# Kernel optimization log

Hardware: AMD Instinct MI355X
Metric: run time of the kernel (lower is better)

The kernel has to match this reference:

```python
import jax, jax.numpy as jnp
import numpy as np
from jax import lax

DIM = 128
N_WORD = 10000
N_FP = 100000
WINDOW = 5
KS = 2 * WINDOW + 1
L_GNN = 3
L_CNN = 3
L_OUT = 2
B, N_ATOM, L_PROT = 64, 256, 2048


def setup_inputs() -> dict:
    key = jax.random.key(0)
    ks = jax.random.split(key, 20)
    s = 0.1  # weight scale (module uses a custom weights_init; any small init is fine)
    return {
        "fingerprints": jax.random.randint(ks[0], (B, N_ATOM), 0, N_FP),
        "adjacency": jax.random.uniform(ks[1], (B, N_ATOM, N_ATOM), jnp.float32),
        "words": jax.random.randint(ks[2], (B, L_PROT), 0, N_WORD),
        "cmask": jnp.ones((B, N_ATOM), jnp.float32),
        "pmask": jnp.ones((B, L_PROT), jnp.float32),
        "label": jax.random.normal(ks[3], (B, 1), jnp.float32),
        "emb_fp": jax.random.normal(ks[4], (N_FP, DIM), jnp.float32) * s,
        "emb_word": jax.random.normal(ks[5], (N_WORD, DIM), jnp.float32) * s,
        "Wg": jax.random.normal(ks[6], (L_GNN, DIM, DIM), jnp.float32) * s,
        "bg": jax.random.normal(ks[7], (L_GNN, DIM), jnp.float32) * s,
        "Wc": jax.random.normal(ks[8], (L_CNN, 1, 1, KS, KS), jnp.float32) * s,
        "bc": jax.random.normal(ks[9], (L_CNN,), jnp.float32) * s,
        "Wa": jax.random.normal(ks[10], (DIM, DIM), jnp.float32) * s,
        "ba": jax.random.normal(ks[11], (DIM,), jnp.float32) * s,
        "Wo": jax.random.normal(ks[12], (L_OUT, 2 * DIM, 2 * DIM), jnp.float32) * s,
        "bo": jax.random.normal(ks[13], (L_OUT, 2 * DIM), jnp.float32) * s,
        "Wi": jax.random.normal(ks[14], (1, 2 * DIM), jnp.float32) * s,
        "bi": jax.random.normal(ks[15], (1,), jnp.float32) * s,
    }


def _conv2d(x, k, b):
    # x: [B,1,L,D], k: [1,1,KS,KS] -> same-padded conv, scalar bias
    y = lax.conv_general_dilated(x, k, (1, 1), [(WINDOW, WINDOW), (WINDOW, WINDOW)],
                                 dimension_numbers=("NCHW", "OIHW", "NCHW"))
    return y + b


def reference(fingerprints, adjacency, words, cmask, pmask, label,
              emb_fp, emb_word, Wg, bg, Wc, bc, Wa, ba, Wo, bo, Wi, bi):
    # --- GNN over compound graph ---
    xs = emb_fp[fingerprints]                          # [B,N,D]
    for i in range(L_GNN):
        hs = jax.nn.relu(jnp.einsum("bnd,ed->bne", xs, Wg[i]) + bg[i])
        xs = xs + jnp.matmul(adjacency, hs)            # residual message passing
    cm = cmask[:, :, None]
    compound = jnp.sum(xs * cm, axis=1) / jnp.sum(cm, axis=1)   # [B,D]

    # --- attention-CNN over protein words ---
    wv = emb_word[words]                               # [B,L,D]
    x4 = wv[:, None, :, :]                             # [B,1,L,D]
    for i in range(L_CNN):
        x4 = jax.nn.relu(_conv2d(x4, Wc[i], bc[i]))
    xs_p = x4[:, 0]                                    # [B,L,D]
    h = jax.nn.relu(compound @ Wa.T + ba)              # [B,D]
    hs = jax.nn.relu(jnp.einsum("bld,ed->ble", xs_p, Wa) + ba)  # [B,L,D]
    weights = jnp.tanh(jnp.einsum("bld,bd->bl", hs, h))[:, :, None]  # [B,L,1]
    ys = weights * hs
    pm = pmask[:, :, None]
    protein = jnp.sum(ys * pm, axis=1) / jnp.sum(pm, axis=1)    # [B,D]

    # --- output head ---
    cat = jnp.concatenate([compound, protein], axis=1)  # [B,2D]
    for j in range(L_OUT):
        cat = jax.nn.relu(cat @ Wo[j].T + bo[j])
    affinity = cat @ Wi.T + bi                           # [B,1]
    loss = jnp.mean((affinity - label) ** 2)             # MSELoss, weight 1
    return (loss, affinity)
```

## Files before the change

kernel.cpp:

```cpp
#include <hip/hip_runtime.h>
#include <hip/hip_bf16.h>
#include <math.h>

#define DIM   128
#define NA    256
#define NB    64
#define LPROT 2048
#define KSZ   11

#define TROWS   64
#define NTILES  (LPROT / TROWS)
#define FRS     152
#define XRS     136
#define B0_ROWS 106
#define B1_ROWS 96

typedef __attribute__((ext_vector_type(8))) short short8v;
typedef __attribute__((ext_vector_type(4))) short short4v;
typedef __attribute__((ext_vector_type(4))) float float4v;

__device__ inline unsigned short f2bf(float f) {
  __hip_bfloat16 h = __float2bfloat16(f);
  unsigned short u; __builtin_memcpy(&u, &h, 2); return u;
}
__device__ inline float bf2f(unsigned short s) {
  union { unsigned u; float f; } v; v.u = ((unsigned)s) << 16;
  return v.f;
}
__device__ inline short8v cvt8(const float* p) {
  float4 x = *(const float4*)p, y = *(const float4*)(p + 4);
  short8v t;
  t[0] = (short)f2bf(x.x); t[1] = (short)f2bf(x.y);
  t[2] = (short)f2bf(x.z); t[3] = (short)f2bf(x.w);
  t[4] = (short)f2bf(y.x); t[5] = (short)f2bf(y.y);
  t[6] = (short)f2bf(y.z); t[7] = (short)f2bf(y.w);
  return t;
}

#define HSTR 512
#define WSTR 256
__device__ inline int hta(int e, int nb) { return (e * HSTR + nb) ^ ((e & 7) << 4); }
__device__ inline int wga(int e, int cb) { return (e * WSTR + cb) ^ ((e & 7) << 4); }

__global__ __launch_bounds__(256) void k_cvtA(const float* __restrict__ A,
                                              unsigned short* __restrict__ Abf) {
  long i = ((long)blockIdx.x * 256 + threadIdx.x) * 8;
  *(short8v*)(Abf + i) = cvt8(A + i);
}

__global__ void k_prepw(const float* __restrict__ Wc, long* __restrict__ wbf) {
  int t = threadIdx.x;
  int lp = t >> 6, lane = t & 63;
  int lj = lane & 15, k0 = (lane >> 4) * 8;
  int bbase = 15 + k0 - lj;
  for (int ki = 0; ki < KSZ; ++ki) {
    float wr[8];
    #pragma unroll
    for (int i = 0; i < 8; ++i) {
      int t2 = bbase + i - 18;
      wr[i] = (t2 >= 0 && t2 < KSZ) ? Wc[lp * KSZ * KSZ + ki * KSZ + t2] : 0.f;
    }
    int lo = __builtin_amdgcn_cvt_pk_fp8_f32(wr[0], wr[1], 0, false);
    lo = __builtin_amdgcn_cvt_pk_fp8_f32(wr[2], wr[3], lo, true);
    int hi = __builtin_amdgcn_cvt_pk_fp8_f32(wr[4], wr[5], 0, false);
    hi = __builtin_amdgcn_cvt_pk_fp8_f32(wr[6], wr[7], hi, true);
    wbf[(lp * 64 + lane) * KSZ + ki] = ((long)hi << 32) | (unsigned)lo;
  }
}

template <bool GATHER>
__global__ __launch_bounds__(512, 2) void k_hs(const float* __restrict__ xs_in,
                                               const int* __restrict__ fp,
                                               const float* __restrict__ emb,
                                               const float* __restrict__ Wgl,
                                               const float* __restrict__ bgl,
                                               unsigned short* __restrict__ hsT) {
  __shared__ __align__(16) char wgp[128 * WSTR];
  const int blk = blockIdx.x, b = blk >> 2, q = blk & 3;
  const int tid = threadIdx.x, lane = tid & 63, w = tid >> 6;
  const int lj = lane & 15, g = lane >> 4, k0 = g * 8;

  for (int i = tid; i < 128 * 16; i += 512) {
    int row = i >> 4, c8 = (i & 15) * 8;
    *(short8v*)(wgp + wga(row, c8 * 2)) = cvt8(&Wgl[row * DIM + c8]);
  }

  const int rrow = q * 64 + (w >> 1) * 16 + lj;
  const int c0 = (w & 1) * 64;

  short8v afr[4];
  {
    const float* src;
    if (GATHER) src = &emb[(long)fp[b * NA + rrow] * DIM];
    else        src = &xs_in[((long)b * NA + rrow) * DIM];
    #pragma unroll
    for (int ks = 0; ks < 4; ++ks) afr[ks] = cvt8(src + ks * 32 + k0);
  }
  __syncthreads();

  float4v acc[4];
  #pragma unroll
  for (int c = 0; c < 4; ++c) acc[c] = (float4v){0.f, 0.f, 0.f, 0.f};
  #pragma unroll
  for (int ks = 0; ks < 4; ++ks)
    #pragma unroll
    for (int c = 0; c < 4; ++c) {
      short8v bf = *(const short8v*)(wgp + wga(c0 + c * 16 + lj, ks * 64 + g * 16));
      acc[c] = __builtin_amdgcn_mfma_f32_16x16x32_bf16(afr[ks], bf, acc[c], 0, 0, 0);
    }

  const int n0 = q * 64 + (w >> 1) * 16 + g * 4;
  #pragma unroll
  for (int c = 0; c < 4; ++c) {
    int e = c0 + c * 16 + lj;
    float bias = bgl[e];
    short4v s;
    #pragma unroll
    for (int jj = 0; jj < 4; ++jj)
      s[jj] = (short)f2bf(fmaxf(acc[c][jj] + bias, 0.f));
    *(short4v*)&hsT[((long)b * DIM + e) * NA + n0] = s;
  }
}

template <bool GATHER, bool LAST>
__global__ __launch_bounds__(512, 2) void k_adj(const float* __restrict__ xs_in,
                                                const int* __restrict__ fp,
                                                const float* __restrict__ emb,
                                                const unsigned short* __restrict__ Abf,
                                                const unsigned short* __restrict__ hsT,
                                                const float* __restrict__ cmask,
                                                float* __restrict__ xs_out,
                                                float* __restrict__ cred) {
  __shared__ __align__(16) char hl[128 * HSTR];
  const int blk = blockIdx.x, b = blk >> 2, q = blk & 3;
  const int tid = threadIdx.x, lane = tid & 63, w = tid >> 6;
  const int lj = lane & 15, g = lane >> 4, k0 = g * 8;

  for (int i = tid; i < 128 * 32; i += 512) {
    int row = i >> 5, c8 = (i & 31) * 8;
    *(short8v*)(hl + hta(row, c8 * 2)) =
        *(const short8v*)&hsT[((long)b * DIM + row) * NA + c8];
  }
  __syncthreads();

  const int wr = w >> 2, wc = w & 3;
  const int row0 = q * 64 + wr * 32;

  float4v acc[2][2];
  #pragma unroll
  for (int m = 0; m < 2; ++m)
    #pragma unroll
    for (int c = 0; c < 2; ++c) acc[m][c] = (float4v){0.f, 0.f, 0.f, 0.f};

  #pragma unroll 2
  for (int ks = 0; ks < 8; ++ks) {
    short8v af0 = *(const short8v*)
        &Abf[((long)b * NA + row0 + lj) * NA + ks * 32 + k0];
    short8v af1 = *(const short8v*)
        &Abf[((long)b * NA + row0 + 16 + lj) * NA + ks * 32 + k0];
    #pragma unroll
    for (int c = 0; c < 2; ++c) {
      short8v bf = *(const short8v*)(hl + hta(wc * 32 + c * 16 + lj, ks * 64 + g * 16));
      acc[0][c] = __builtin_amdgcn_mfma_f32_16x16x32_bf16(af0, bf, acc[0][c], 0, 0, 0);
      acc[1][c] = __builtin_amdgcn_mfma_f32_16x16x32_bf16(af1, bf, acc[1][c], 0, 0, 0);
    }
  }

  if (!LAST) {
    #pragma unroll
    for (int m = 0; m < 2; ++m)
      #pragma unroll
      for (int jj = 0; jj < 4; ++jj) {
        int row = row0 + m * 16 + g * 4 + jj;
        long base = ((long)b * NA + row) * DIM;
        const float* oldsrc;
        long gbase;
        if (GATHER) { gbase = (long)fp[b * NA + row] * DIM; oldsrc = emb; }
        else { gbase = base; oldsrc = xs_in; }
        #pragma unroll
        for (int c = 0; c < 2; ++c) {
          int col = wc * 32 + c * 16 + lj;
          xs_out[base + col] = oldsrc[gbase + col] + acc[m][c][jj];
        }
      }
  } else {
    float p[2] = {0.f, 0.f};
    #pragma unroll
    for (int m = 0; m < 2; ++m)
      #pragma unroll
      for (int jj = 0; jj < 4; ++jj) {
        int row = row0 + m * 16 + g * 4 + jj;
        float cm = cmask[b * NA + row];
        long base = ((long)b * NA + row) * DIM;
        #pragma unroll
        for (int c = 0; c < 2; ++c) {
          int col = wc * 32 + c * 16 + lj;
          float xv = xs_in[base + col] + acc[m][c][jj];
          p[c] = fmaf(xv, cm, p[c]);
        }
      }
    #pragma unroll
    for (int c = 0; c < 2; ++c) {
      p[c] += __shfl_xor(p[c], 16);
      p[c] += __shfl_xor(p[c], 32);
      if (g == 0)
        cred[((long)b * 8 + q * 2 + wr) * DIM + wc * 32 + c * 16 + lj] = p[c];
    }
  }
}

__global__ __launch_bounds__(128) void k_hv(const float* __restrict__ cred,
                                            const float* __restrict__ cmask,
                                            const float* __restrict__ Wa,
                                            const float* __restrict__ ba,
                                            float* __restrict__ compound,
                                            float* __restrict__ hv) {
  int b = blockIdx.x, e = threadIdx.x;
  __shared__ float comp[DIM];
  __shared__ float redm[DIM];
  float s = 0.f;
  #pragma unroll
  for (int p = 0; p < 8; ++p) s += cred[((long)b * 8 + p) * DIM + e];
  redm[e] = cmask[b * NA + e] + cmask[b * NA + DIM + e];
  __syncthreads();
  for (int st = 64; st > 0; st >>= 1) {
    if (e < st) redm[e] += redm[e + st];
    __syncthreads();
  }
  float c = s / redm[0];
  compound[b * DIM + e] = c;
  comp[e] = c;
  __syncthreads();
  float acc = 0.f;
  for (int d = 0; d < DIM; d += 4) {
    float4 wv = *(const float4*)&Wa[e * DIM + d];
    float4 x  = *(const float4*)&comp[d];
    acc = fmaf(x.x, wv.x, fmaf(x.y, wv.y, fmaf(x.z, wv.z, fmaf(x.w, wv.w, acc))));
  }
  hv[b * DIM + e] = fmaxf(acc + ba[e], 0.f);
}

template <bool ROWCHK, bool BF16OUT>
__device__ inline void conv_epi(const float4v& acc, int rc,
                                char* __restrict__ dst,
                                unsigned short* __restrict__ dstX,
                                float bias, int dstart, int lane, int cc) {
  const int lj = lane & 15;
  int orow = rc * 16 + (lane >> 4) * 4;
  int ocol = cc * 16 + lj;
  #pragma unroll
  for (int jj = 0; jj < 4; ++jj) {
    float v = fmaxf(acc[jj] + bias, 0.f);
    if constexpr (BF16OUT) {
      dstX[(orow + jj) * XRS + ocol] = f2bf(v);
    } else {
      char sv = 0;
      if (!ROWCHK || (unsigned)(dstart + orow + jj) < LPROT) {
        int p = __builtin_amdgcn_cvt_pk_fp8_f32(v, 0.f, 0, false);
        sv = (char)p;
      }
      dst[(orow + jj) * FRS + 8 + ocol] = sv;
    }
  }
}

template <int N_RC, bool ROWCHK, bool BF16OUT>
__device__ inline void conv_fp8(const char* __restrict__ src, char* __restrict__ dst,
                                unsigned short* __restrict__ dstX,
                                const long* bfr, float bias, int dstart,
                                int lane, int cc) {
  const int lj = lane & 15, k0 = (lane >> 4) * 8;
  const int acol = 8 + cc * 16 + k0;
  #pragma unroll 1
  for (int rp = 0; rp < N_RC / 2; ++rp) {
    const int rc0 = rp * 2, rc1 = rc0 + 1;
    float4v acc0 = {0.f, 0.f, 0.f, 0.f};
    float4v acc1 = {0.f, 0.f, 0.f, 0.f};
    #pragma unroll
    for (int ki = 0; ki < KSZ; ++ki) {
      long a0 = *(const long*)(src + (rc0 * 16 + lj + ki) * FRS + acol);
      long a1 = *(const long*)(src + (rc1 * 16 + lj + ki) * FRS + acol);
      acc0 = __builtin_amdgcn_mfma_f32_16x16x32_fp8_fp8(a0, bfr[ki], acc0, 0, 0, 0);
      acc1 = __builtin_amdgcn_mfma_f32_16x16x32_fp8_fp8(a1, bfr[ki], acc1, 0, 0, 0);
    }
    conv_epi<ROWCHK, BF16OUT>(acc0, rc0, dst, dstX, bias, dstart, lane, cc);
    conv_epi<ROWCHK, BF16OUT>(acc1, rc1, dst, dstX, bias, dstart, lane, cc);
  }
  if (N_RC & 1) {
    const int rc = N_RC - 1;
    float4v acc = {0.f, 0.f, 0.f, 0.f};
    #pragma unroll
    for (int ki = 0; ki < KSZ; ++ki) {
      long a = *(const long*)(src + (rc * 16 + lj + ki) * FRS + acol);
      acc = __builtin_amdgcn_mfma_f32_16x16x32_fp8_fp8(a, bfr[ki], acc, 0, 0, 0);
    }
    conv_epi<ROWCHK, BF16OUT>(acc, rc, dst, dstX, bias, dstart, lane, cc);
  }
}

__global__ __launch_bounds__(512, 6) void k_protein(const int* __restrict__ words,
                                                    const float* __restrict__ emb_word,
                                                    const long* __restrict__ wbf,
                                                    const float* __restrict__ bc,
                                                    const float* __restrict__ Wa,
                                                    const float* __restrict__ ba,
                                                    const float* __restrict__ hvec,
                                                    const float* __restrict__ pmask,
                                                    float* __restrict__ prot_part) {
  __shared__ __align__(16) char pool[48640];
  char* buf0 = pool;
  char* buf1 = pool + 16128;
  unsigned short* bufX = (unsigned short*)(pool + 30720);
  float* h_s  = (float*)(pool + 48128);
  float* wpart = (float*)(pool + 16128);
  float* w_l   = (float*)(pool + 16128 + 2048);
  float* red   = (float*)(pool + 16128 + 2304);

  const int tile = blockIdx.x, b = blockIdx.y;
  const int r0   = tile * TROWS;
  const int tid  = threadIdx.x;
  const int lane = tid & 63, wave = tid >> 6;
  const int lj   = lane & 15;
  const int k0   = (lane >> 4) * 8;
  const int cc   = wave;

  {
    int4 z = {0, 0, 0, 0};
    int4* p0 = (int4*)pool;
    for (int i = tid; i < 30720 / 16; i += 512) p0[i] = z;
  }
  if (tid < DIM) h_s[tid] = hvec[b * DIM + tid];

  for (int idx = tid; idx < B0_ROWS * 32; idx += 512) {
    int rloc = idx >> 5, c4 = idx & 31;
    int rg = r0 - 15 + rloc;
    if (rg >= 0 && rg < LPROT) {
      int w = words[b * LPROT + rg];
      float4 v = ((const float4*)(emb_word + (long)w * DIM))[c4];
      int p = __builtin_amdgcn_cvt_pk_fp8_f32(v.x, v.y, 0, false);
      p = __builtin_amdgcn_cvt_pk_fp8_f32(v.z, v.w, p, true);
      *(int*)(buf0 + rloc * FRS + 8 + c4 * 4) = p;
    }
  }

  #pragma unroll 1
  for (int lp = 0; lp < 3; ++lp) {
    __syncthreads();
    long bfr[KSZ];
    const long* wsrc = wbf + (lp * 64 + lane) * KSZ;
    #pragma unroll
    for (int ki = 0; ki < KSZ; ++ki) bfr[ki] = wsrc[ki];
    float bias = bc[lp];

    if (lp == 0)
      conv_fp8<6, true, false>(buf0, buf1, nullptr, bfr, bias, r0 - 10, lane, cc);
    else if (lp == 1)
      conv_fp8<5, true, false>(buf1, buf0, nullptr, bfr, bias, r0 - 5, lane, cc);
    else
      conv_fp8<4, false, true>(buf0, nullptr, bufX, bfr, bias, r0, lane, cc);
  }
  __syncthreads();

  {
    const char* xb = (const char*)bufX;
    float4v acc[4];
    #pragma unroll
    for (int rc = 0; rc < 4; ++rc) acc[rc] = (float4v){0.f, 0.f, 0.f, 0.f};
    #pragma unroll
    for (int ks = 0; ks < 4; ++ks) {
      const float* wrow = Wa + (cc * 16 + lj) * DIM + ks * 32 + k0;
      short8v bf = cvt8(wrow);
      #pragma unroll
      for (int rc = 0; rc < 4; ++rc) {
        short8v a = *(const short8v*)(xb + (rc * 16 + lj) * (XRS * 2) + (ks * 32 + k0) * 2);
        acc[rc] = __builtin_amdgcn_mfma_f32_16x16x32_bf16(a, bf, acc[rc], 0, 0, 0);
      }
    }
    __syncthreads();
    float bav = ba[cc * 16 + lj];
    #pragma unroll
    for (int rc = 0; rc < 4; ++rc) {
      int orow = rc * 16 + (lane >> 4) * 4;
      int ocol = cc * 16 + lj;
      #pragma unroll
      for (int jj = 0; jj < 4; ++jj) {
        float v = fmaxf(acc[rc][jj] + bav, 0.f);
        bufX[(orow + jj) * XRS + ocol] = f2bf(v);
      }
    }
  }
  __syncthreads();

  {
    int l = tid >> 3, part = tid & 7, d0 = part * 16;
    short8v v0 = *(const short8v*)&bufX[l * XRS + d0];
    short8v v1 = *(const short8v*)&bufX[l * XRS + d0 + 8];
    float4 h0 = *(const float4*)&h_s[d0];
    float4 h1 = *(const float4*)&h_s[d0 + 4];
    float4 h2 = *(const float4*)&h_s[d0 + 8];
    float4 h3 = *(const float4*)&h_s[d0 + 12];
    float s = 0.f;
    s = fmaf(bf2f((unsigned short)v0[0]), h0.x, s);
    s = fmaf(bf2f((unsigned short)v0[1]), h0.y, s);
    s = fmaf(bf2f((unsigned short)v0[2]), h0.z, s);
    s = fmaf(bf2f((unsigned short)v0[3]), h0.w, s);
    s = fmaf(bf2f((unsigned short)v0[4]), h1.x, s);
    s = fmaf(bf2f((unsigned short)v0[5]), h1.y, s);
    s = fmaf(bf2f((unsigned short)v0[6]), h1.z, s);
    s = fmaf(bf2f((unsigned short)v0[7]), h1.w, s);
    s = fmaf(bf2f((unsigned short)v1[0]), h2.x, s);
    s = fmaf(bf2f((unsigned short)v1[1]), h2.y, s);
    s = fmaf(bf2f((unsigned short)v1[2]), h2.z, s);
    s = fmaf(bf2f((unsigned short)v1[3]), h2.w, s);
    s = fmaf(bf2f((unsigned short)v1[4]), h3.x, s);
    s = fmaf(bf2f((unsigned short)v1[5]), h3.y, s);
    s = fmaf(bf2f((unsigned short)v1[6]), h3.z, s);
    s = fmaf(bf2f((unsigned short)v1[7]), h3.w, s);
    wpart[l * 8 + part] = s;
  }
  __syncthreads();
  if (tid < TROWS) {
    float s = 0.f;
    #pragma unroll
    for (int p = 0; p < 8; ++p) s += wpart[tid * 8 + p];
    w_l[tid] = tanhf(s) * pmask[b * LPROT + r0 + tid];
  }
  __syncthreads();

  {
    int e = tid & 127, g = tid >> 7;
    float s = 0.f;
    #pragma unroll
    for (int j = 0; j < 16; ++j) {
      int l = g * 16 + j;
      s = fmaf(w_l[l], bf2f(bufX[l * XRS + e]), s);
    }
    red[g * DIM + e] = s;
  }
  __syncthreads();
  if (tid < DIM)
    prot_part[((long)b * NTILES + tile) * DIM + tid] =
        red[tid] + red[DIM + tid] + red[2 * DIM + tid] + red[3 * DIM + tid];
}

__global__ __launch_bounds__(256) void k_head(const float* __restrict__ prot_part,
                                              const float* __restrict__ pmask,
                                              const float* __restrict__ compound,
                                              const float* __restrict__ Wo,
                                              const float* __restrict__ bo,
                                              const float* __restrict__ Wi,
                                              const float* __restrict__ bi,
                                              float* __restrict__ out) {
  int b = blockIdx.x, tid = threadIdx.x;
  __shared__ float cat[2 * DIM];
  __shared__ float redl[256];

  float ps = 0.f;
  for (int l = tid; l < LPROT; l += 256) ps += pmask[b * LPROT + l];
  redl[tid] = ps; __syncthreads();
  for (int st = 128; st > 0; st >>= 1) {
    if (tid < st) redl[tid] += redl[tid + st];
    __syncthreads();
  }
  float pden = redl[0];
  __syncthreads();

  if (tid < DIM) {
    cat[tid] = compound[b * DIM + tid];
    float s = 0.f;
    for (int t = 0; t < NTILES; ++t) s += prot_part[(b * NTILES + t) * DIM + tid];
    cat[DIM + tid] = s / pden;
  }
  __syncthreads();

  for (int j = 0; j < 2; ++j) {
    const float* W = Wo + j * 2 * DIM * 2 * DIM + tid * 2 * DIM;
    float acc = 0.f;
    for (int d = 0; d < 2 * DIM; d += 4) {
      float4 c = *(const float4*)&cat[d];
      float4 w = *(const float4*)&W[d];
      acc = fmaf(c.x, w.x, fmaf(c.y, w.y, fmaf(c.z, w.z, fmaf(c.w, w.w, acc))));
    }
    float v = fmaxf(acc + bo[j * 2 * DIM + tid], 0.f);
    __syncthreads();
    cat[tid] = v;
    __syncthreads();
  }

  float p = cat[tid] * Wi[tid];
  redl[tid] = p; __syncthreads();
  for (int st = 128; st > 0; st >>= 1) {
    if (tid < st) redl[tid] += redl[tid + st];
    __syncthreads();
  }
  if (tid == 0) out[1 + b] = redl[0] + bi[0];
}

__global__ void k_loss(const float* __restrict__ label, float* __restrict__ out) {
  int t = threadIdx.x;
  float d = out[1 + t] - label[t];
  float v = d * d;
  #pragma unroll
  for (int s = 32; s > 0; s >>= 1) v += __shfl_down(v, s);
  if (t == 0) out[0] = v * (1.f / 64.f);
}

extern "C" void kernel_launch(void* const* d_in, const int* in_sizes, int n_in,
                              void* d_out, int out_size, void* d_ws, size_t ws_size,
                              hipStream_t stream) {
  const int*   fingerprints = (const int*)d_in[0];
  const float* adjacency    = (const float*)d_in[1];
  const int*   words        = (const int*)d_in[2];
  const float* cmask        = (const float*)d_in[3];
  const float* pmask        = (const float*)d_in[4];
  const float* label        = (const float*)d_in[5];
  const float* emb_fp       = (const float*)d_in[6];
  const float* emb_word     = (const float*)d_in[7];
  const float* Wg           = (const float*)d_in[8];
  const float* bg           = (const float*)d_in[9];
  const float* Wc           = (const float*)d_in[10];
  const float* bc           = (const float*)d_in[11];
  const float* Wa           = (const float*)d_in[12];
  const float* ba           = (const float*)d_in[13];
  const float* Wo           = (const float*)d_in[14];
  const float* bo           = (const float*)d_in[15];
  const float* Wi           = (const float*)d_in[16];
  const float* bi           = (const float*)d_in[17];
  float* out = (float*)d_out;

  unsigned short* Abf = (unsigned short*)d_ws;
  float* xs = (float*)(Abf + (long)NB * NA * NA);
  unsigned short* hsT = (unsigned short*)(xs + NB * NA * DIM);
  float* cred = (float*)(hsT + (long)NB * DIM * NA);
  float* compound  = cred + NB * 8 * DIM;
  float* hv        = compound + NB * DIM;
  float* prot_part = hv + NB * DIM;
  long*  wbf       = (long*)(prot_part + NB * NTILES * DIM);

  k_cvtA<<<(NB * NA * NA) / (256 * 8), 256, 0, stream>>>(adjacency, Abf);
  k_prepw<<<1, 192, 0, stream>>>(Wc, wbf);

  k_hs<true><<<256, 512, 0, stream>>>(nullptr, fingerprints, emb_fp, Wg, bg, hsT);
  k_adj<true, false><<<256, 512, 0, stream>>>(nullptr, fingerprints, emb_fp,
                                              Abf, hsT, nullptr, xs, nullptr);
  k_hs<false><<<256, 512, 0, stream>>>(xs, nullptr, nullptr, Wg + DIM * DIM,
                                       bg + DIM, hsT);
  k_adj<false, false><<<256, 512, 0, stream>>>(xs, nullptr, nullptr,
                                               Abf, hsT, nullptr, xs, nullptr);
  k_hs<false><<<256, 512, 0, stream>>>(xs, nullptr, nullptr, Wg + 2 * DIM * DIM,
                                       bg + 2 * DIM, hsT);
  k_adj<false, true><<<256, 512, 0, stream>>>(xs, nullptr, nullptr,
                                              Abf, hsT, cmask, nullptr, cred);
  k_hv<<<NB, 128, 0, stream>>>(cred, cmask, Wa, ba, compound, hv);

  k_protein<<<dim3(NTILES, NB), 512, 0, stream>>>(words, emb_word, wbf, bc, Wa, ba,
                                                  hv, pmask, prot_part);
  k_head<<<NB, 256, 0, stream>>>(prot_part, pmask, compound, Wo, bo, Wi, bi, out);
  k_loss<<<1, 64, 0, stream>>>(label, out);
}
```

Measured before the change: 153.8 us.

## Fuse GNN hs and adjacency kernels per layer, merge prep kernels, shrink protein LDS

```diff
diff --git a/kernel.cpp b/kernel.cpp
--- a/kernel.cpp
+++ b/kernel.cpp
@@ -39,107 +39,102 @@
 
 #define HSTR 512
 #define WSTR 256
+__device__ inline int xsa(int n, int cb) { return (n * 256 + cb) ^ ((n & 7) << 4); }
 __device__ inline int hta(int e, int nb) { return (e * HSTR + nb) ^ ((e & 7) << 4); }
 __device__ inline int wga(int e, int cb) { return (e * WSTR + cb) ^ ((e & 7) << 4); }
 
-__global__ __launch_bounds__(256) void k_cvtA(const float* __restrict__ A,
-                                              unsigned short* __restrict__ Abf) {
-  long i = ((long)blockIdx.x * 256 + threadIdx.x) * 8;
-  *(short8v*)(Abf + i) = cvt8(A + i);
-}
-
-__global__ void k_prepw(const float* __restrict__ Wc, long* __restrict__ wbf) {
-  int t = threadIdx.x;
-  int lp = t >> 6, lane = t & 63;
-  int lj = lane & 15, k0 = (lane >> 4) * 8;
-  int bbase = 15 + k0 - lj;
-  for (int ki = 0; ki < KSZ; ++ki) {
-    float wr[8];
-    #pragma unroll
-    for (int i = 0; i < 8; ++i) {
-      int t2 = bbase + i - 18;
-      wr[i] = (t2 >= 0 && t2 < KSZ) ? Wc[lp * KSZ * KSZ + ki * KSZ + t2] : 0.f;
-    }
-    int lo = __builtin_amdgcn_cvt_pk_fp8_f32(wr[0], wr[1], 0, false);
-    lo = __builtin_amdgcn_cvt_pk_fp8_f32(wr[2], wr[3], lo, true);
-    int hi = __builtin_amdgcn_cvt_pk_fp8_f32(wr[4], wr[5], 0, false);
-    hi = __builtin_amdgcn_cvt_pk_fp8_f32(wr[6], wr[7], hi, true);
-    wbf[(lp * 64 + lane) * KSZ + ki] = ((long)hi << 32) | (unsigned)lo;
-  }
-}
-
-template <bool GATHER>
-__global__ __launch_bounds__(512, 2) void k_hs(const float* __restrict__ xs_in,
-                                               const int* __restrict__ fp,
-                                               const float* __restrict__ emb,
-                                               const float* __restrict__ Wgl,
-                                               const float* __restrict__ bgl,
-                                               unsigned short* __restrict__ hsT) {
-  __shared__ __align__(16) char wgp[128 * WSTR];
+__global__ __launch_bounds__(256) void k_pre(const float* __restrict__ A,
+                                             unsigned short* __restrict__ Abf,
+                                             const float* __restrict__ Wc,
+                                             long* __restrict__ wbf) {
+  int blk = blockIdx.x;
+  if (blk < 2048) {
+    long i = ((long)blk * 256 + threadIdx.x) * 8;
+    *(short8v*)(Abf + i) = cvt8(A + i);
+  } else if (threadIdx.x < 192) {
+    int t = threadIdx.x;
+    int lp = t >> 6, lane = t & 63;
+    int lj = lane & 15, k0 = (lane >> 4) * 8;
+    int bbase = 15 + k0 - lj;
+    for (int ki = 0; ki < KSZ; ++ki) {
+      float wr[8];
+      #pragma unroll
+      for (int i = 0; i < 8; ++i) {
+        int t2 = bbase + i - 18;
+        wr[i] = (t2 >= 0 && t2 < KSZ) ? Wc[lp * KSZ * KSZ + ki * KSZ + t2] : 0.f;
+      }
+      int lo = __builtin_amdgcn_cvt_pk_fp8_f32(wr[0], wr[1], 0, false);
+      lo = __builtin_amdgcn_cvt_pk_fp8_f32(wr[2], wr[3], lo, true);
+      int hi = __builtin_amdgcn_cvt_pk_fp8_f32(wr[4], wr[5], 0, false);
+      hi = __builtin_amdgcn_cvt_pk_fp8_f32(wr[6], wr[7], hi, true);
+      wbf[(lp * 64 + lane) * KSZ + ki] = ((long)hi << 32) | (unsigned)lo;
+    }
+  }
+}
+
+template <bool GATHER, bool LAST>
+__global__ __launch_bounds__(512, 1) void k_layer(
+    const float* __restrict__ xs_in,
+    const int* __restrict__ fp,
+    const float* __restrict__ emb,
+    const unsigned short* __restrict__ Abf,
+    const float* __restrict__ Wg,
+    const float* __restrict__ bg,
+    const float* __restrict__ cmask,
+    float* __restrict__ xs_out,
+    float* __restrict__ cred) {
+  __shared__ __align__(16) char pool[98304];
+  char* reg0 = pool;
+  char* wgp  = pool + 65536;
+
   const int blk = blockIdx.x, b = blk >> 2, q = blk & 3;
   const int tid = threadIdx.x, lane = tid & 63, w = tid >> 6;
   const int lj = lane & 15, g = lane >> 4, k0 = g * 8;
 
   for (int i = tid; i < 128 * 16; i += 512) {
     int row = i >> 4, c8 = (i & 15) * 8;
-    *(short8v*)(wgp + wga(row, c8 * 2)) = cvt8(&Wgl[row * DIM + c8]);
-  }
-
-  const int rrow = q * 64 + (w >> 1) * 16 + lj;
-  const int c0 = (w & 1) * 64;
-
-  short8v afr[4];
-  {
-    const float* src;
-    if (GATHER) src = &emb[(long)fp[b * NA + rrow] * DIM];
-    else        src = &xs_in[((long)b * NA + rrow) * DIM];
-    #pragma unroll
-    for (int ks = 0; ks < 4; ++ks) afr[ks] = cvt8(src + ks * 32 + k0);
-  }
-  __syncthreads();
-
-  float4v acc[4];
-  #pragma unroll
-  for (int c = 0; c < 4; ++c) acc[c] = (float4v){0.f, 0.f, 0.f, 0.f};
-  #pragma unroll
-  for (int ks = 0; ks < 4; ++ks)
-    #pragma unroll
-    for (int c = 0; c < 4; ++c) {
-      short8v bf = *(const short8v*)(wgp + wga(c0 + c * 16 + lj, ks * 64 + g * 16));
-      acc[c] = __builtin_amdgcn_mfma_f32_16x16x32_bf16(afr[ks], bf, acc[c], 0, 0, 0);
-    }
-
-  const int n0 = q * 64 + (w >> 1) * 16 + g * 4;
-  #pragma unroll
-  for (int c = 0; c < 4; ++c) {
-    int e = c0 + c * 16 + lj;
-    float bias = bgl[e];
-    short4v s;
-    #pragma unroll
-    for (int jj = 0; jj < 4; ++jj)
-      s[jj] = (short)f2bf(fmaxf(acc[c][jj] + bias, 0.f));
-    *(short4v*)&hsT[((long)b * DIM + e) * NA + n0] = s;
-  }
-}
-
-template <bool GATHER, bool LAST>
-__global__ __launch_bounds__(512, 2) void k_adj(const float* __restrict__ xs_in,
-                                                const int* __restrict__ fp,
-                                                const float* __restrict__ emb,
-                                                const unsigned short* __restrict__ Abf,
-                                                const unsigned short* __restrict__ hsT,
-                                                const float* __restrict__ cmask,
-                                                float* __restrict__ xs_out,
-                                                float* __restrict__ cred) {
-  __shared__ __align__(16) char hl[128 * HSTR];
-  const int blk = blockIdx.x, b = blk >> 2, q = blk & 3;
-  const int tid = threadIdx.x, lane = tid & 63, w = tid >> 6;
-  const int lj = lane & 15, g = lane >> 4, k0 = g * 8;
-
-  for (int i = tid; i < 128 * 32; i += 512) {
-    int row = i >> 5, c8 = (i & 31) * 8;
-    *(short8v*)(hl + hta(row, c8 * 2)) =
-        *(const short8v*)&hsT[((long)b * DIM + row) * NA + c8];
+    *(short8v*)(wgp + wga(row, c8 * 2)) = cvt8(&Wg[row * DIM + c8]);
+  }
+  for (int i = tid; i < 256 * 16; i += 512) {
+    int r = i >> 4, c8 = (i & 15) * 8;
+    const float* src = GATHER ? &emb[(long)fp[b * NA + r] * DIM + c8]
+                              : &xs_in[((long)b * NA + r) * DIM + c8];
+    *(short8v*)(reg0 + xsa(r, c8 * 2)) = cvt8(src);
+  }
+  __syncthreads();
+
+  const int rbase = w * 32;
+  float4v hacc[2][8];
+  #pragma unroll
+  for (int m = 0; m < 2; ++m)
+    #pragma unroll
+    for (int c = 0; c < 8; ++c) hacc[m][c] = (float4v){0.f, 0.f, 0.f, 0.f};
+  #pragma unroll
+  for (int ks = 0; ks < 4; ++ks) {
+    short8v a0 = *(const short8v*)(reg0 + xsa(rbase + lj,      ks * 64 + g * 16));
+    short8v a1 = *(const short8v*)(reg0 + xsa(rbase + 16 + lj, ks * 64 + g * 16));
+    #pragma unroll
+    for (int c = 0; c < 8; ++c) {
+      short8v bf = *(const short8v*)(wgp + wga(c * 16 + lj, ks * 64 + g * 16));
+      hacc[0][c] = __builtin_amdgcn_mfma_f32_16x16x32_bf16(a0, bf, hacc[0][c], 0, 0, 0);
+      hacc[1][c] = __builtin_amdgcn_mfma_f32_16x16x32_bf16(a1, bf, hacc[1][c], 0, 0, 0);
+    }
+  }
+  __syncthreads();
+
+  #pragma unroll
+  for (int m = 0; m < 2; ++m) {
+    int n0 = rbase + m * 16 + g * 4;
+    #pragma unroll
+    for (int c = 0; c < 8; ++c) {
+      int e = c * 16 + lj;
+      float bias = bg[e];
+      short4v s;
+      #pragma unroll
+      for (int jj = 0; jj < 4; ++jj)
+        s[jj] = (short)f2bf(fmaxf(hacc[m][c][jj] + bias, 0.f));
+      *(short4v*)(reg0 + hta(e, n0 * 2)) = s;
+    }
   }
   __syncthreads();
 
@@ -160,7 +155,7 @@
         &Abf[((long)b * NA + row0 + 16 + lj) * NA + ks * 32 + k0];
     #pragma unroll
     for (int c = 0; c < 2; ++c) {
-      short8v bf = *(const short8v*)(hl + hta(wc * 32 + c * 16 + lj, ks * 64 + g * 16));
+      short8v bf = *(const short8v*)(reg0 + hta(wc * 32 + c * 16 + lj, ks * 64 + g * 16));
       acc[0][c] = __builtin_amdgcn_mfma_f32_16x16x32_bf16(af0, bf, acc[0][c], 0, 0, 0);
       acc[1][c] = __builtin_amdgcn_mfma_f32_16x16x32_bf16(af1, bf, acc[1][c], 0, 0, 0);
     }
@@ -298,7 +293,7 @@
   }
 }
 
-__global__ __launch_bounds__(512, 6) void k_protein(const int* __restrict__ words,
+__global__ __launch_bounds__(512, 8) void k_protein(const int* __restrict__ words,
                                                     const float* __restrict__ emb_word,
                                                     const long* __restrict__ wbf,
                                                     const float* __restrict__ bc,
@@ -307,14 +302,14 @@
                                                     const float* __restrict__ hvec,
                                                     const float* __restrict__ pmask,
                                                     float* __restrict__ prot_part) {
-  __shared__ __align__(16) char pool[48640];
+  __shared__ __align__(16) char pool[38400];
   char* buf0 = pool;
   char* buf1 = pool + 16128;
-  unsigned short* bufX = (unsigned short*)(pool + 30720);
-  float* h_s  = (float*)(pool + 48128);
-  float* wpart = (float*)(pool + 16128);
-  float* w_l   = (float*)(pool + 16128 + 2048);
-  float* red   = (float*)(pool + 16128 + 2304);
+  unsigned short* bufX = (unsigned short*)(pool + 16128);
+  float* wpart = (float*)(pool + 33536);
+  float* w_l   = (float*)(pool + 35584);
+  float* red   = (float*)(pool + 35840);
+  float* h_s   = (float*)(pool + 37888);
 
   const int tile = blockIdx.x, b = blockIdx.y;
   const int r0   = tile * TROWS;
@@ -529,28 +524,23 @@
   float* out = (float*)d_out;
 
   unsigned short* Abf = (unsigned short*)d_ws;
-  float* xs = (float*)(Abf + (long)NB * NA * NA);
-  unsigned short* hsT = (unsigned short*)(xs + NB * NA * DIM);
-  float* cred = (float*)(hsT + (long)NB * DIM * NA);
+  float* xs1 = (float*)(Abf + (long)NB * NA * NA);
+  float* xs2 = xs1 + (long)NB * NA * DIM;
+  float* cred = xs2 + (long)NB * NA * DIM;
   float* compound  = cred + NB * 8 * DIM;
   float* hv        = compound + NB * DIM;
   float* prot_part = hv + NB * DIM;
   long*  wbf       = (long*)(prot_part + NB * NTILES * DIM);
 
-  k_cvtA<<<(NB * NA * NA) / (256 * 8), 256, 0, stream>>>(adjacency, Abf);
-  k_prepw<<<1, 192, 0, stream>>>(Wc, wbf);
-
-  k_hs<true><<<256, 512, 0, stream>>>(nullptr, fingerprints, emb_fp, Wg, bg, hsT);
-  k_adj<true, false><<<256, 512, 0, stream>>>(nullptr, fingerprints, emb_fp,
-                                              Abf, hsT, nullptr, xs, nullptr);
-  k_hs<false><<<256, 512, 0, stream>>>(xs, nullptr, nullptr, Wg + DIM * DIM,
-                                       bg + DIM, hsT);
-  k_adj<false, false><<<256, 512, 0, stream>>>(xs, nullptr, nullptr,
-                                               Abf, hsT, nullptr, xs, nullptr);
-  k_hs<false><<<256, 512, 0, stream>>>(xs, nullptr, nullptr, Wg + 2 * DIM * DIM,
-                                       bg + 2 * DIM, hsT);
-  k_adj<false, true><<<256, 512, 0, stream>>>(xs, nullptr, nullptr,
-                                              Abf, hsT, cmask, nullptr, cred);
+  k_pre<<<2049, 256, 0, stream>>>(adjacency, Abf, Wc, wbf);
+
+  k_layer<true,  false><<<256, 512, 0, stream>>>(
+      nullptr, fingerprints, emb_fp, Abf, Wg, bg, nullptr, xs1, nullptr);
+  k_layer<false, false><<<256, 512, 0, stream>>>(
+      xs1, nullptr, nullptr, Abf, Wg + DIM * DIM, bg + DIM, nullptr, xs2, nullptr);
+  k_layer<false, true><<<256, 512, 0, stream>>>(
+      xs2, nullptr, nullptr, Abf, Wg + 2 * DIM * DIM, bg + 2 * DIM,
+      cmask, nullptr, cred);
   k_hv<<<NB, 128, 0, stream>>>(cred, cmask, Wa, ba, compound, hv);
 
   k_protein<<<dim3(NTILES, NB), 512, 0, stream>>>(words, emb_word, wbf, bc, Wa, ba,
```

Result: faster. 141.0 us (-8.3%).
